# Kernel optimization log

Measured on AMD Instinct MI355X. Metric: run time of the kernel, lower is better.

Reference implementation:

```python
import jax, jax.numpy as jnp
import numpy as np

H = 64        # hidden dim (all layers)
L = 6         # number of AdaLN layers
TE = 32       # time embed dim
SEL = 64      # selection dim
CD = 128      # cond dim
DC = 128      # context feature dim
EPS = 1e-6    # flax LayerNorm default epsilon


def swish(x):
    return x * jax.nn.sigmoid(x)


def time_embedding(t, dim=TE):
    # standard sinusoidal time embedding; t: (B,1) -> (B,dim)
    half = dim // 2
    freqs = jnp.exp(-jnp.log(10000.0) * jnp.arange(half, dtype=jnp.float32) / (half - 1))
    args = t * freqs[None, :]
    return jnp.concatenate([jnp.sin(args), jnp.cos(args)], axis=-1)


def layernorm(x, g, b):
    mu = jnp.mean(x, axis=-1, keepdims=True)
    xc = x - mu
    var = jnp.mean(xc * xc, axis=-1, keepdims=True)
    return xc * jax.lax.rsqrt(var + EPS) * g + b


def forward(x, c, t, W_emb, b_emb, W_pf, b_pf, W_of, b_of, W_c1, b_c1,
            W_c2, b_c2, W_h, b_h, W_ss, b_ss, ln_g, ln_b, W_out, b_out):
    B, N, D = x.shape
    K = c.shape[1]
    t_feat = time_embedding(t[:, None])                     # (B,TE)
    x_embed = x @ W_emb + b_emb                             # (B,N,H)
    point_features = swish(x_embed @ W_pf + b_pf)           # (B,N,SEL)
    c_with_time = jnp.concatenate(
        [jnp.broadcast_to(t_feat[:, None, :], (B, K, TE)), c], axis=-1)  # (B,K,TE+DC)
    object_features = swish(c_with_time @ W_of + b_of)      # (B,K,SEL)
    affinity = jnp.einsum('bnd,bkd->bnk', point_features, object_features)
    selection_weights = jax.nn.softmax(affinity, axis=-1)   # (B,N,K)
    cond_objects = swish(swish(c_with_time @ W_c1 + b_c1) @ W_c2 + b_c2)  # (B,K,CD)
    cond = jnp.einsum('bnk,bkd->bnd', selection_weights, cond_objects)    # (B,N,CD)

    h = swish(x_embed)

    def body(h, p):
        W, b, Wss, bss, g, bln = p
        h = swish(h @ W + b)                                # (B,N,H)
        scale_shift = cond @ Wss + bss                      # (B,N,2H)
        scale, shift = jnp.split(scale_shift, 2, axis=-1)
        h = layernorm(h, g, bln)
        h = h * (1.0 + scale) + shift
        return h, None

    h, _ = jax.lax.scan(body, h, (W_h, b_h, W_ss, b_ss, ln_g, ln_b))
    dx = h @ W_out + b_out                                  # (B,N,D)
    return dx


def setup_inputs() -> dict:
    key = jax.random.key(0)
    ks = jax.random.split(key, 16)
    B, N, D, K = 32, 8192, 3, 16
    s = 0.02
    inp = {
        'x': jax.random.normal(ks[0], (B, N, D), jnp.float32),
        'c': jax.random.normal(ks[1], (B, K, DC), jnp.float32),
        't': jax.random.uniform(ks[2], (B,), jnp.float32),
        'W_emb': s * jax.random.normal(ks[3], (D, H), jnp.float32),
        'b_emb': jnp.zeros((H,), jnp.float32),
        'W_pf': s * jax.random.normal(ks[4], (H, SEL), jnp.float32),
        'b_pf': jnp.zeros((SEL,), jnp.float32),
        'W_of': s * jax.random.normal(ks[5], (TE + DC, SEL), jnp.float32),
        'b_of': jnp.zeros((SEL,), jnp.float32),
        'W_c1': s * jax.random.normal(ks[6], (TE + DC, CD), jnp.float32),
        'b_c1': jnp.zeros((CD,), jnp.float32),
        'W_c2': s * jax.random.normal(ks[7], (CD, CD), jnp.float32),
        'b_c2': jnp.zeros((CD,), jnp.float32),
        'W_h': s * jax.random.normal(ks[8], (L, H, H), jnp.float32),
        'b_h': jnp.zeros((L, H), jnp.float32),
        'W_ss': s * jax.random.normal(ks[9], (L, CD, 2 * H), jnp.float32),
        'b_ss': jnp.zeros((L, 2 * H), jnp.float32),
        'ln_g': jnp.ones((L, H), jnp.float32),
        'ln_b': jnp.zeros((L, H), jnp.float32),
        'W_out': s * jax.random.normal(ks[10], (H, D), jnp.float32),
        'b_out': jnp.zeros((D,), jnp.float32),
    }
    return inp


def reference(x, c, t, W_emb, b_emb, W_pf, b_pf, W_of, b_of, W_c1, b_c1,
              W_c2, b_c2, W_h, b_h, W_ss, b_ss, ln_g, ln_b, W_out, b_out):
    return forward(x, c, t, W_emb, b_emb, W_pf, b_pf, W_of, b_of, W_c1, b_c1,
                   W_c2, b_c2, W_h, b_h, W_ss, b_ss, ln_g, ln_b, W_out, b_out)
```

## Files before the change

kernel.cpp:

```cpp
#include <hip/hip_runtime.h>
#include <hip/hip_bf16.h>
#include <math.h>

#define H   64
#define L   6
#define TE  32
#define SEL 64
#define CD  128
#define DC  128
#define KK  16
#define BB  32
#define NN  8192
#define EPSV 1e-6f

typedef float f32x4  __attribute__((ext_vector_type(4)));
typedef short bf16x8 __attribute__((ext_vector_type(8)));
typedef short bf16x4 __attribute__((ext_vector_type(4)));

__device__ __forceinline__ float swish_f(float v) {
    return v * __builtin_amdgcn_rcpf(1.0f + __expf(-v));
}
__device__ __forceinline__ short f2bf(float f) {
    __hip_bfloat16 h = __float2bfloat16(f);
    return *reinterpret_cast<short*>(&h);
}

#if __has_builtin(__builtin_amdgcn_permlane16_swap) && __has_builtin(__builtin_amdgcn_permlane32_swap)
__device__ __forceinline__ float red_add64(float x) {
    auto r16 = __builtin_amdgcn_permlane16_swap(__float_as_uint(x), __float_as_uint(x), false, false);
    float s = __uint_as_float(r16[0]) + __uint_as_float(r16[1]);
    auto r32 = __builtin_amdgcn_permlane32_swap(__float_as_uint(s), __float_as_uint(s), false, false);
    return __uint_as_float(r32[0]) + __uint_as_float(r32[1]);
}
__device__ __forceinline__ float red_max64(float x) {
    auto r16 = __builtin_amdgcn_permlane16_swap(__float_as_uint(x), __float_as_uint(x), false, false);
    float s = fmaxf(__uint_as_float(r16[0]), __uint_as_float(r16[1]));
    auto r32 = __builtin_amdgcn_permlane32_swap(__float_as_uint(s), __float_as_uint(s), false, false);
    return fmaxf(__uint_as_float(r32[0]), __uint_as_float(r32[1]));
}
#else
__device__ __forceinline__ float red_add64(float x) {
    x += __shfl_xor(x, 16);
    x += __shfl_xor(x, 32);
    return x;
}
__device__ __forceinline__ float red_max64(float x) {
    x = fmaxf(x, __shfl_xor(x, 16));
    x = fmaxf(x, __shfl_xor(x, 32));
    return x;
}
#endif

#if __has_builtin(__builtin_amdgcn_mfma_f32_16x16x16bf16_1k)
#define MFMA16(a, b, c) __builtin_amdgcn_mfma_f32_16x16x16bf16_1k(a, b, c, 0, 0, 0)
#else
__device__ __forceinline__ f32x4 mfma16_asm(bf16x4 a, bf16x4 b, f32x4 c) {
    f32x4 d;
    asm("v_mfma_f32_16x16x16_bf16 %0, %1, %2, %3" : "=&v"(d) : "v"(a), "v"(b), "v"(c));
    return d;
}
#define MFMA16(a, b, c) mfma16_asm(a, b, c)
#endif
#define MFMA32(a, b, c) __builtin_amdgcn_mfma_f32_16x16x32_bf16(a, b, c, 0, 0, 0)

#define OFF_OBJF 0
#define OFF_TAB  32768
#define OFF_WH   425984
#define OFF_WPF  450560

__global__ void setup_w(const float* __restrict__ W_h, const float* __restrict__ W_pf,
                        short* __restrict__ whfrag, short* __restrict__ wpffrag) {
    const int gid = blockIdx.x * 256 + threadIdx.x;
    for (int idx = gid; idx < 6 * 4 * 2 * 64 * 8; idx += 8192) {
        const int jj = idx & 7, lane = (idx >> 3) & 63, s = (idx >> 9) & 1,
                  t = (idx >> 10) & 3, l = idx >> 12;
        const int g = lane >> 4, row = 16 * t + (lane & 15), k = 32 * s + 8 * g + jj;
        whfrag[idx] = f2bf(W_h[(l * H + k) * H + row]);
    }
    for (int idx = gid; idx < 4 * 2 * 64 * 8; idx += 8192) {
        const int jj = idx & 7, lane = (idx >> 3) & 63, s = (idx >> 9) & 1, t = idx >> 10;
        const int g = lane >> 4, row = 16 * t + (lane & 15), k = 32 * s + 8 * g + jj;
        wpffrag[idx] = f2bf(W_pf[k * SEL + row]);
    }
}

__global__ void setup_obj(const float* __restrict__ c, const float* __restrict__ t,
                          const float* __restrict__ W_of, const float* __restrict__ b_of,
                          const float* __restrict__ W_c1, const float* __restrict__ b_c1,
                          const float* __restrict__ W_c2, const float* __restrict__ b_c2,
                          const float* __restrict__ W_ss, const float* __restrict__ b_ss,
                          short* __restrict__ objffrag, short* __restrict__ tabfrag) {
    const int bk = blockIdx.x, b = bk >> 4, k = bk & 15;
    const int tid = threadIdx.x;
    __shared__ float cwt[TE + DC];
    __shared__ float c1s[CD], c2s[CD];

    if (tid < 16) {
        float f   = __expf(-logf(10000.0f) * (float)tid * (1.0f / 15.0f));
        float arg = t[b] * f;
        cwt[tid]      = sinf(arg);
        cwt[tid + 16] = cosf(arg);
    }
    cwt[TE + tid] = c[(b * KK + k) * DC + tid];
    __syncthreads();

    if (tid < SEL) {
        float a = b_of[tid];
        for (int d = 0; d < TE + DC; ++d) a += cwt[d] * W_of[d * SEL + tid];
        a = swish_f(a);
        const int s = tid >> 5, g = (tid >> 3) & 3, jj = tid & 7;
        objffrag[(((b * 2 + s) * 64) + (16 * g + k)) * 8 + jj] = f2bf(a);
    }
    {
        float a = b_c1[tid];
        for (int d = 0; d < TE + DC; ++d) a += cwt[d] * W_c1[d * CD + tid];
        c1s[tid] = swish_f(a);
    }
    __syncthreads();
    {
        float a = b_c2[tid];
        for (int d = 0; d < CD; ++d) a += c1s[d] * W_c2[d * CD + tid];
        c2s[tid] = swish_f(a);
    }
    __syncthreads();

    const int u = tid >> 4, row = tid & 15, lane = 16 * (k >> 2) + row, jj = k & 3;
    for (int l = 0; l < L; ++l) {
        const float* W = W_ss + l * CD * (2 * H);
        float a = b_ss[l * (2 * H) + tid];
        for (int d = 0; d < CD; ++d) a += c2s[d] * W[d * (2 * H) + tid];
        tabfrag[(((b * 6 + l) * 8 + u) * 64 + lane) * 4 + jj] = f2bf(a);
    }
}

__global__ __launch_bounds__(256, 3) void main_kernel(
    const float* __restrict__ x,
    const float* __restrict__ W_emb, const float* __restrict__ b_emb,
    const float* __restrict__ b_pf,  const float* __restrict__ b_h,
    const float* __restrict__ ln_g,  const float* __restrict__ ln_b,
    const float* __restrict__ W_out, const float* __restrict__ b_out,
    const short* __restrict__ objffrag, const short* __restrict__ tabfrag,
    const short* __restrict__ whfrag,   const short* __restrict__ wpffrag,
    float* __restrict__ out) {

    __shared__ short hlds[128 * 72];

    const int tid  = threadIdx.x;
    const int wave = tid >> 6, lane = tid & 63;
    const int p = lane & 15, g = lane >> 4;
    const int b = blockIdx.x >> 6;
    const int point0 = (blockIdx.x & 63) << 7;

    bf16x8 wpfr[4][2], objr[2];
#pragma unroll
    for (int t = 0; t < 4; ++t)
#pragma unroll
        for (int s = 0; s < 2; ++s)
            wpfr[t][s] = *(const bf16x8*)&wpffrag[(((t * 2 + s) * 64) + lane) * 8];
#pragma unroll
    for (int s = 0; s < 2; ++s)
        objr[s] = *(const bf16x8*)&objffrag[(((b * 2 + s) * 64) + lane) * 8];

    bf16x4 swfrag[2];

#pragma unroll
    for (int i = 0; i < 2; ++i) {
        const int tloc = (wave * 2 + i) * 16 + p;
        const int ptg  = b * NN + point0 + tloc;
        const float x0 = x[ptg * 3 + 0], x1 = x[ptg * 3 + 1], x2 = x[ptg * 3 + 2];

        float  ev[2][8];
        bf16x8 eb[2];
#pragma unroll
        for (int s = 0; s < 2; ++s)
#pragma unroll
            for (int jj = 0; jj < 8; ++jj) {
                const int k = 32 * s + 8 * g + jj;
                float e = b_emb[k] + x0 * W_emb[k] + x1 * W_emb[H + k] + x2 * W_emb[2 * H + k];
                ev[s][jj] = e;
                eb[s][jj] = f2bf(e);
            }

        f32x4 macc[4];
#pragma unroll
        for (int t = 0; t < 4; ++t) {
            const float4 bp = *(const float4*)&b_pf[16 * t + 4 * g];
            f32x4 m; m[0] = bp.x; m[1] = bp.y; m[2] = bp.z; m[3] = bp.w;
            m = MFMA32(wpfr[t][0], eb[0], m);
            m = MFMA32(wpfr[t][1], eb[1], m);
            macc[t] = m;
        }
#pragma unroll
        for (int t = 0; t < 4; ++t) {
            short4 w;
            w.x = f2bf(swish_f(macc[t][0]));
            w.y = f2bf(swish_f(macc[t][1]));
            w.z = f2bf(swish_f(macc[t][2]));
            w.w = f2bf(swish_f(macc[t][3]));
            *(short4*)&hlds[tloc * 72 + 16 * t + 4 * g] = w;
        }
        bf16x8 pfb[2];
#pragma unroll
        for (int s = 0; s < 2; ++s)
            pfb[s] = *(bf16x8*)&hlds[tloc * 72 + 32 * s + 8 * g];

        f32x4 aacc = {0.f, 0.f, 0.f, 0.f};
#pragma unroll
        for (int s = 0; s < 2; ++s)
            aacc = MFMA32(objr[s], pfb[s], aacc);

        const float mx = red_max64(fmaxf(fmaxf(aacc[0], aacc[1]), fmaxf(aacc[2], aacc[3])));
        float swv[4], ssl = 0.f;
#pragma unroll
        for (int r = 0; r < 4; ++r) { swv[r] = __expf(aacc[r] - mx); ssl += swv[r]; }
        const float inv = __builtin_amdgcn_rcpf(red_add64(ssl));

        bf16x4 sf;
#pragma unroll
        for (int r = 0; r < 4; ++r) sf[r] = f2bf(swv[r] * inv);
        swfrag[i] = sf;

#pragma unroll
        for (int s = 0; s < 2; ++s) {
            bf16x8 hb;
#pragma unroll
            for (int jj = 0; jj < 8; ++jj) hb[jj] = f2bf(swish_f(ev[s][jj]));
            *(bf16x8*)&hlds[tloc * 72 + 32 * s + 8 * g] = hb;
        }
    }

    for (int l = 0; l < L; ++l) {
        bf16x8 whr[4][2];
        bf16x4 tabr[8];
#pragma unroll
        for (int t = 0; t < 4; ++t)
#pragma unroll
            for (int s = 0; s < 2; ++s)
                whr[t][s] = *(const bf16x8*)&whfrag[((l * 8 + t * 2 + s) * 64 + lane) * 8];
#pragma unroll
        for (int u = 0; u < 8; ++u)
            tabr[u] = *(const bf16x4*)&tabfrag[(((b * 6 + l) * 8 + u) * 64 + lane) * 4];

#pragma unroll
        for (int i = 0; i < 2; ++i) {
            const int tloc = (wave * 2 + i) * 16 + p;
            const bf16x8 hb0 = *(bf16x8*)&hlds[tloc * 72 + 8 * g];
            const bf16x8 hb1 = *(bf16x8*)&hlds[tloc * 72 + 32 + 8 * g];
            const bf16x4 sf  = swfrag[i];

            f32x4 sca[4];
#pragma unroll
            for (int u = 0; u < 4; ++u) {
                f32x4 z = {0.f, 0.f, 0.f, 0.f};
                sca[u] = MFMA16(tabr[u], sf, z);
            }

            f32x4 macc[4];
#pragma unroll
            for (int t = 0; t < 4; ++t) {
                const float4 bh = *(const float4*)&b_h[l * H + 16 * t + 4 * g];
                f32x4 m; m[0] = bh.x; m[1] = bh.y; m[2] = bh.z; m[3] = bh.w;
                m = MFMA32(whr[t][0], hb0, m);
                m = MFMA32(whr[t][1], hb1, m);
                macc[t] = m;
            }

            float hn[4][4], s1 = 0.f, s2 = 0.f;
#pragma unroll
            for (int t = 0; t < 4; ++t)
#pragma unroll
                for (int r = 0; r < 4; ++r) {
                    const float v = swish_f(macc[t][r]);
                    hn[t][r] = v; s1 += v; s2 += v * v;
                }
            s1 = red_add64(s1);
            s2 = red_add64(s2);
            const float mu  = s1 * (1.0f / 64.0f);
            const float var = s2 * (1.0f / 64.0f) - mu * mu;
            const float rin = rsqrtf(var + EPSV);

            f32x4 sha[4];
#pragma unroll
            for (int u = 0; u < 4; ++u) {
                f32x4 z = {0.f, 0.f, 0.f, 0.f};
                sha[u] = MFMA16(tabr[4 + u], sf, z);
            }

            if (l < L - 1) {
#pragma unroll
                for (int t = 0; t < 4; ++t) {
                    const float4 gg = *(const float4*)&ln_g[l * H + 16 * t + 4 * g];
                    const float4 bb = *(const float4*)&ln_b[l * H + 16 * t + 4 * g];
                    float ggv[4]; ggv[0] = gg.x; ggv[1] = gg.y; ggv[2] = gg.z; ggv[3] = gg.w;
                    float bbv[4]; bbv[0] = bb.x; bbv[1] = bb.y; bbv[2] = bb.z; bbv[3] = bb.w;
                    short wv[4];
#pragma unroll
                    for (int r = 0; r < 4; ++r) {
                        const float lnv = (hn[t][r] - mu) * rin * ggv[r] + bbv[r];
                        wv[r] = f2bf(lnv * (1.0f + sca[t][r]) + sha[t][r]);
                    }
                    short4 w; w.x = wv[0]; w.y = wv[1]; w.z = wv[2]; w.w = wv[3];
                    *(short4*)&hlds[tloc * 72 + 16 * t + 4 * g] = w;
                }
            } else {
                float d0 = 0.f, d1 = 0.f, d2 = 0.f;
#pragma unroll
                for (int t = 0; t < 4; ++t) {
                    const float4 gg = *(const float4*)&ln_g[l * H + 16 * t + 4 * g];
                    const float4 bb = *(const float4*)&ln_b[l * H + 16 * t + 4 * g];
                    float ggv[4]; ggv[0] = gg.x; ggv[1] = gg.y; ggv[2] = gg.z; ggv[3] = gg.w;
                    float bbv[4]; bbv[0] = bb.x; bbv[1] = bb.y; bbv[2] = bb.z; bbv[3] = bb.w;
                    const float4 w0 = *(const float4*)&W_out[(16 * t + 4 * g) * 3];
                    const float4 w1 = *(const float4*)&W_out[(16 * t + 4 * g) * 3 + 4];
                    const float4 w2 = *(const float4*)&W_out[(16 * t + 4 * g) * 3 + 8];
                    float wv[12];
                    wv[0] = w0.x; wv[1] = w0.y; wv[2]  = w0.z; wv[3]  = w0.w;
                    wv[4] = w1.x; wv[5] = w1.y; wv[6]  = w1.z; wv[7]  = w1.w;
                    wv[8] = w2.x; wv[9] = w2.y; wv[10] = w2.z; wv[11] = w2.w;
#pragma unroll
                    for (int r = 0; r < 4; ++r) {
                        const float lnv = (hn[t][r] - mu) * rin * ggv[r] + bbv[r];
                        const float hv  = lnv * (1.0f + sca[t][r]) + sha[t][r];
                        d0 += hv * wv[r * 3 + 0];
                        d1 += hv * wv[r * 3 + 1];
                        d2 += hv * wv[r * 3 + 2];
                    }
                }
                d0 = red_add64(d0);
                d1 = red_add64(d1);
                d2 = red_add64(d2);
                if (g == 0) {
                    const int ptg = b * NN + point0 + tloc;
                    out[ptg * 3 + 0] = d0 + b_out[0];
                    out[ptg * 3 + 1] = d1 + b_out[1];
                    out[ptg * 3 + 2] = d2 + b_out[2];
                }
            }
        }
    }
}

extern "C" void kernel_launch(void* const* d_in, const int* in_sizes, int n_in,
                              void* d_out, int out_size, void* d_ws, size_t ws_size,
                              hipStream_t stream) {
    const float* x     = (const float*)d_in[0];
    const float* c     = (const float*)d_in[1];
    const float* t     = (const float*)d_in[2];
    const float* W_emb = (const float*)d_in[3];
    const float* b_emb = (const float*)d_in[4];
    const float* W_pf  = (const float*)d_in[5];
    const float* b_pf  = (const float*)d_in[6];
    const float* W_of  = (const float*)d_in[7];
    const float* b_of  = (const float*)d_in[8];
    const float* W_c1  = (const float*)d_in[9];
    const float* b_c1  = (const float*)d_in[10];
    const float* W_c2  = (const float*)d_in[11];
    const float* b_c2  = (const float*)d_in[12];
    const float* W_h   = (const float*)d_in[13];
    const float* b_h   = (const float*)d_in[14];
    const float* W_ss  = (const float*)d_in[15];
    const float* b_ss  = (const float*)d_in[16];
    const float* ln_g  = (const float*)d_in[17];
    const float* ln_b  = (const float*)d_in[18];
    const float* W_out = (const float*)d_in[19];
    const float* b_out = (const float*)d_in[20];
    float* out = (float*)d_out;

    short* wsb      = (short*)d_ws;
    short* objffrag = wsb + OFF_OBJF;
    short* tabfrag  = wsb + OFF_TAB;
    short* whfrag   = wsb + OFF_WH;
    short* wpffrag  = wsb + OFF_WPF;

    setup_w<<<32, 256, 0, stream>>>(W_h, W_pf, whfrag, wpffrag);
    setup_obj<<<BB * KK, 128, 0, stream>>>(c, t, W_of, b_of, W_c1, b_c1,
                                           W_c2, b_c2, W_ss, b_ss, objffrag, tabfrag);
    main_kernel<<<2048, 256, 0, stream>>>(x, W_emb, b_emb, b_pf, b_h, ln_g, ln_b,
                                          W_out, b_out, objffrag, tabfrag,
                                          whfrag, wpffrag, out);
}
```

Baseline: 113.1 us.

## Merge setup kernels into one launch and raise main kernel occupancy bound

Merges the weight-fragment conversion kernel and the per-object setup kernel into a single launch. Blocks beyond index 512 handle the weight conversion, and the object blocks now run 256 threads with half of them idle behind guards. This removes one kernel launch and its inter-kernel gap. The main kernel's launch bounds minimum-blocks hint goes from 3 to 4, which may force fewer registers per thread and risks spills.

```diff
diff --git a/kernel.cpp b/kernel.cpp
--- a/kernel.cpp
+++ b/kernel.cpp
@@ -68,28 +68,30 @@
 #define OFF_WH   425984
 #define OFF_WPF  450560
 
-__global__ void setup_w(const float* __restrict__ W_h, const float* __restrict__ W_pf,
-                        short* __restrict__ whfrag, short* __restrict__ wpffrag) {
-    const int gid = blockIdx.x * 256 + threadIdx.x;
-    for (int idx = gid; idx < 6 * 4 * 2 * 64 * 8; idx += 8192) {
-        const int jj = idx & 7, lane = (idx >> 3) & 63, s = (idx >> 9) & 1,
-                  t = (idx >> 10) & 3, l = idx >> 12;
-        const int g = lane >> 4, row = 16 * t + (lane & 15), k = 32 * s + 8 * g + jj;
-        whfrag[idx] = f2bf(W_h[(l * H + k) * H + row]);
-    }
-    for (int idx = gid; idx < 4 * 2 * 64 * 8; idx += 8192) {
-        const int jj = idx & 7, lane = (idx >> 3) & 63, s = (idx >> 9) & 1, t = idx >> 10;
-        const int g = lane >> 4, row = 16 * t + (lane & 15), k = 32 * s + 8 * g + jj;
-        wpffrag[idx] = f2bf(W_pf[k * SEL + row]);
-    }
-}
-
-__global__ void setup_obj(const float* __restrict__ c, const float* __restrict__ t,
+__global__ void setup_all(const float* __restrict__ c, const float* __restrict__ t,
                           const float* __restrict__ W_of, const float* __restrict__ b_of,
                           const float* __restrict__ W_c1, const float* __restrict__ b_c1,
                           const float* __restrict__ W_c2, const float* __restrict__ b_c2,
                           const float* __restrict__ W_ss, const float* __restrict__ b_ss,
-                          short* __restrict__ objffrag, short* __restrict__ tabfrag) {
+                          const float* __restrict__ W_h,  const float* __restrict__ W_pf,
+                          short* __restrict__ objffrag, short* __restrict__ tabfrag,
+                          short* __restrict__ whfrag,   short* __restrict__ wpffrag) {
+    if (blockIdx.x >= 512) {
+        const int gid = (blockIdx.x - 512) * 256 + threadIdx.x;
+        for (int idx = gid; idx < 6 * 4 * 2 * 64 * 8; idx += 8192) {
+            const int jj = idx & 7, lane = (idx >> 3) & 63, s = (idx >> 9) & 1,
+                      tt = (idx >> 10) & 3, l = idx >> 12;
+            const int g = lane >> 4, row = 16 * tt + (lane & 15), k = 32 * s + 8 * g + jj;
+            whfrag[idx] = f2bf(W_h[(l * H + k) * H + row]);
+        }
+        for (int idx = gid; idx < 4 * 2 * 64 * 8; idx += 8192) {
+            const int jj = idx & 7, lane = (idx >> 3) & 63, s = (idx >> 9) & 1, tt = idx >> 10;
+            const int g = lane >> 4, row = 16 * tt + (lane & 15), k = 32 * s + 8 * g + jj;
+            wpffrag[idx] = f2bf(W_pf[k * SEL + row]);
+        }
+        return;
+    }
+
     const int bk = blockIdx.x, b = bk >> 4, k = bk & 15;
     const int tid = threadIdx.x;
     __shared__ float cwt[TE + DC];
@@ -101,7 +103,7 @@
         cwt[tid]      = sinf(arg);
         cwt[tid + 16] = cosf(arg);
     }
-    cwt[TE + tid] = c[(b * KK + k) * DC + tid];
+    if (tid < 128) cwt[TE + tid] = c[(b * KK + k) * DC + tid];
     __syncthreads();
 
     if (tid < SEL) {
@@ -111,29 +113,31 @@
         const int s = tid >> 5, g = (tid >> 3) & 3, jj = tid & 7;
         objffrag[(((b * 2 + s) * 64) + (16 * g + k)) * 8 + jj] = f2bf(a);
     }
-    {
+    if (tid < 128) {
         float a = b_c1[tid];
         for (int d = 0; d < TE + DC; ++d) a += cwt[d] * W_c1[d * CD + tid];
         c1s[tid] = swish_f(a);
     }
     __syncthreads();
-    {
+    if (tid < 128) {
         float a = b_c2[tid];
         for (int d = 0; d < CD; ++d) a += c1s[d] * W_c2[d * CD + tid];
         c2s[tid] = swish_f(a);
     }
     __syncthreads();
 
-    const int u = tid >> 4, row = tid & 15, lane = 16 * (k >> 2) + row, jj = k & 3;
-    for (int l = 0; l < L; ++l) {
-        const float* W = W_ss + l * CD * (2 * H);
-        float a = b_ss[l * (2 * H) + tid];
-        for (int d = 0; d < CD; ++d) a += c2s[d] * W[d * (2 * H) + tid];
-        tabfrag[(((b * 6 + l) * 8 + u) * 64 + lane) * 4 + jj] = f2bf(a);
-    }
-}
-
-__global__ __launch_bounds__(256, 3) void main_kernel(
+    if (tid < 128) {
+        const int u = tid >> 4, row = tid & 15, lane = 16 * (k >> 2) + row, jj = k & 3;
+        for (int l = 0; l < L; ++l) {
+            const float* W = W_ss + l * CD * (2 * H);
+            float a = b_ss[l * (2 * H) + tid];
+            for (int d = 0; d < CD; ++d) a += c2s[d] * W[d * (2 * H) + tid];
+            tabfrag[(((b * 6 + l) * 8 + u) * 64 + lane) * 4 + jj] = f2bf(a);
+        }
+    }
+}
+
+__global__ __launch_bounds__(256, 4) void main_kernel(
     const float* __restrict__ x,
     const float* __restrict__ W_emb, const float* __restrict__ b_emb,
     const float* __restrict__ b_pf,  const float* __restrict__ b_h,
@@ -372,9 +376,9 @@
     short* whfrag   = wsb + OFF_WH;
     short* wpffrag  = wsb + OFF_WPF;
 
-    setup_w<<<32, 256, 0, stream>>>(W_h, W_pf, whfrag, wpffrag);
-    setup_obj<<<BB * KK, 128, 0, stream>>>(c, t, W_of, b_of, W_c1, b_c1,
-                                           W_c2, b_c2, W_ss, b_ss, objffrag, tabfrag);
+    setup_all<<<544, 256, 0, stream>>>(c, t, W_of, b_of, W_c1, b_c1,
+                                       W_c2, b_c2, W_ss, b_ss, W_h, W_pf,
+                                       objffrag, tabfrag, whfrag, wpffrag);
     main_kernel<<<2048, 256, 0, stream>>>(x, W_emb, b_emb, b_pf, b_h, ln_g, ln_b,
                                           W_out, b_out, objffrag, tabfrag,
                                           whfrag, wpffrag, out);
```

Result: slower. 156.6 us (+38.5%).
